# Performance work log

Hardware: AMD Instinct MI355X
Metric: run time of the kernel (lower is better)

The kernel has to match this reference:

```python
import jax, jax.numpy as jnp
import numpy as np

B, V, S, H = 16384, 16, 64, 512


def setup_inputs() -> dict:
    key = jax.random.key(0)
    kx, kw, kb, kws, kbs = jax.random.split(key, 5)
    x = jax.random.normal(kx, (B, V, S), dtype=jnp.float32)
    # per-variable linear layers: weight [V, S, H], bias [V, H]
    W = jax.random.normal(kw, (V, S, H), dtype=jnp.float32) * (1.0 / np.sqrt(S))
    b = jax.random.normal(kb, (V, H), dtype=jnp.float32) * 0.01
    # variable selection linear: hidden -> V
    W_sel = jax.random.normal(kws, (H, V), dtype=jnp.float32) * (1.0 / np.sqrt(H))
    b_sel = jax.random.normal(kbs, (V,), dtype=jnp.float32) * 0.01
    return {"x": x, "W": W, "b": b, "W_sel": W_sel, "b_sel": b_sel}


def reference(x, W, b, W_sel, b_sel):
    # per-variable linears: [B, V, H]
    transformed = jnp.einsum('bvs,vsh->bvh', x, W) + b  # grouped small GEMMs
    # torch stacks to [B, H, V]; mean over variable axis -> [B, H]
    flat = transformed.mean(axis=1)
    # softmax-gated selection weights [B, V] (dropout is identity in eval)
    weights = jax.nn.softmax(flat @ W_sel + b_sel, axis=-1)
    # weighted sum over variables -> [B, H]
    out = jnp.einsum('bvh,bv->bh', transformed, weights)
    return out
```

## Files before the change

kernel.cpp:

```cpp
#include <hip/hip_runtime.h>
#include <hip/hip_bf16.h>
#include <stdint.h>

#define B_ROWS 16384
#define VDIM   16
#define SDIM   64
#define HDIM   512
#define KDIM   1024
#define KP     1056

using bf16x8 = __attribute__((ext_vector_type(8))) __bf16;
using u16x8  = __attribute__((ext_vector_type(8))) unsigned short;
using f32x4  = __attribute__((ext_vector_type(4))) float;

__device__ __forceinline__ unsigned short f2bf(float f) {
  unsigned int u = __builtin_bit_cast(unsigned int, f);
  u = (u + 0x7FFFu + ((u >> 16) & 1u)) >> 16;
  return (unsigned short)u;
}

__device__ __forceinline__ void gl_lds16(const void* g, void* l) {
  __builtin_amdgcn_global_load_lds(
      (const __attribute__((address_space(1))) void*)(g),
      (__attribute__((address_space(3))) void*)(l),
      16, 0, 0);
}

__global__ __launch_bounds__(256) void k0a_build_bt(
    const float* __restrict__ W, const float* __restrict__ bias,
    unsigned short* __restrict__ Bt) {
  int idx = blockIdx.x * 256 + threadIdx.x;
  if (idx >= KP * HDIM) return;
  int k = idx >> 9;
  int n = idx & 511;
  float val;
  if (k < KDIM)            val = W[(size_t)k * HDIM + n];
  else if (k < KDIM + 16)  val = bias[(size_t)(k - KDIM) * HDIM + n];
  else                     val = 0.f;
  Bt[(size_t)n * KP + k] = f2bf(val);
}

__global__ __launch_bounds__(256) void k0b_comb(
    const float* __restrict__ W, const float* __restrict__ bias,
    const float* __restrict__ Wsel, const float* __restrict__ bsel,
    unsigned short* __restrict__ WcombT, float* __restrict__ bcomb) {
  __shared__ float wsl[512 * 17];
  __shared__ float bm[HDIM];
  __shared__ float part[16][17];
  const int t = threadIdx.x;
  if (blockIdx.x < 256) {
    for (int i = t; i < 512 * 16; i += 256) {
      int h = i >> 4, v = i & 15;
      wsl[h * 17 + v] = Wsel[i];
    }
    __syncthreads();
    const int wave = t >> 6, lane = t & 63;
    const int k = blockIdx.x * 4 + wave;
    const float* wr = W + (size_t)k * HDIM;
    float s[16];
    #pragma unroll
    for (int v = 0; v < 16; ++v) s[v] = 0.f;
    #pragma unroll
    for (int j = 0; j < 8; ++j) {
      const int h = lane + 64 * j;
      const float a = wr[h];
      const float* wl = &wsl[h * 17];
      #pragma unroll
      for (int v = 0; v < 16; ++v) s[v] = fmaf(a, wl[v], s[v]);
    }
    #pragma unroll
    for (int off = 32; off > 0; off >>= 1) {
      #pragma unroll
      for (int v = 0; v < 16; ++v) s[v] += __shfl_xor(s[v], off, 64);
    }
    float mine = 0.f;
    #pragma unroll
    for (int v = 0; v < 16; ++v) mine = (lane == v) ? s[v] : mine;
    if (lane < 16) WcombT[lane * KDIM + k] = f2bf(mine * (1.f / 16.f));
  } else {
    for (int h = t; h < HDIM; h += 256) {
      float s = 0.f;
      #pragma unroll
      for (int v = 0; v < VDIM; ++v) s += bias[v * HDIM + h];
      bm[h] = s * (1.f / 16.f);
    }
    __syncthreads();
    int v = t & 15, sl = t >> 4;
    float s = 0.f;
    for (int h = sl * 32; h < sl * 32 + 32; ++h) s = fmaf(bm[h], Wsel[h * VDIM + v], s);
    part[sl][v] = s;
    __syncthreads();
    if (t < 16) {
      float s2 = bsel[t];
      #pragma unroll
      for (int i = 0; i < 16; ++i) s2 += part[i][t];
      bcomb[t] = s2;
    }
  }
}

__global__ __launch_bounds__(256) void k1a_logits(
    const float* __restrict__ x, const unsigned short* __restrict__ WcombT,
    float* __restrict__ part) {
  const int gw = blockIdx.x * 4 + (threadIdx.x >> 6);
  const int lane = threadIdx.x & 63;
  const int rt = gw >> 2, seg = gw & 3;
  const int m = lane & 15, quad = lane >> 4;
  const float* xr = x + (size_t)(rt * 16 + m) * KDIM + seg * 256 + quad * 8;
  const unsigned short* br = WcombT + m * KDIM + seg * 256 + quad * 8;
  f32x4 acc = {0.f, 0.f, 0.f, 0.f};
  #pragma unroll
  for (int kt = 0; kt < 8; ++kt) {
    float4 a0 = *(const float4*)(xr);
    float4 a1 = *(const float4*)(xr + 4);
    xr += 32;
    u16x8 u;
    u[0] = f2bf(a0.x); u[1] = f2bf(a0.y); u[2] = f2bf(a0.z); u[3] = f2bf(a0.w);
    u[4] = f2bf(a1.x); u[5] = f2bf(a1.y); u[6] = f2bf(a1.z); u[7] = f2bf(a1.w);
    bf16x8 af = __builtin_bit_cast(bf16x8, u);
    bf16x8 bfv = *(const bf16x8*)(br);
    br += 32;
    acc = __builtin_amdgcn_mfma_f32_16x16x32_bf16(af, bfv, acc, 0, 0, 0);
  }
  float* pr = part + (size_t)(rt * 16 + quad * 4) * 64 + seg * 16 + m;
  #pragma unroll
  for (int r = 0; r < 4; ++r) pr[(size_t)r * 64] = acc[r];
}

__global__ __launch_bounds__(256) void k1b0_softmax(
    const float* __restrict__ part, const float* __restrict__ bcomb,
    float* __restrict__ weights, unsigned short* __restrict__ Ax) {
  const int row = blockIdx.x * 256 + threadIdx.x;
  const float* p = part + (size_t)row * 64;
  float l[16];
  float mx = -1e30f;
  #pragma unroll
  for (int v = 0; v < 16; ++v) {
    l[v] = bcomb[v] + p[v] + p[16 + v] + p[32 + v] + p[48 + v];
    mx = fmaxf(mx, l[v]);
  }
  float s = 0.f;
  #pragma unroll
  for (int v = 0; v < 16; ++v) { l[v] = __expf(l[v] - mx); s += l[v]; }
  const float inv = 1.f / s;
  float4* wout = (float4*)(weights + (size_t)row * 16);
  #pragma unroll
  for (int q = 0; q < 4; ++q) {
    float4 f;
    f.x = l[4 * q + 0] * inv; f.y = l[4 * q + 1] * inv;
    f.z = l[4 * q + 2] * inv; f.w = l[4 * q + 3] * inv;
    wout[q] = f;
  }
  unsigned short tb[16];
  #pragma unroll
  for (int v = 0; v < 16; ++v) tb[v] = f2bf(l[v] * inv);
  uint4* tp = (uint4*)(Ax + (size_t)row * KP + KDIM);
  tp[0] = *(const uint4*)(&tb[0]);
  tp[1] = *(const uint4*)(&tb[8]);
  uint4 z; z.x = 0; z.y = 0; z.z = 0; z.w = 0;
  tp[2] = z;
  tp[3] = z;
}

__global__ __launch_bounds__(256) void k1b_scale(
    const float* __restrict__ x, const float* __restrict__ weights,
    unsigned short* __restrict__ Ax) {
  const int wave = threadIdx.x >> 6, lane = threadIdx.x & 63;
  #pragma unroll
  for (int r = 0; r < 2; ++r) {
    const int row = blockIdx.x * 8 + wave * 2 + r;
    const float w = weights[(size_t)row * 16 + (lane >> 2)];
    const float4* xr = (const float4*)(x + (size_t)row * KDIM + lane * 16);
    float4 v0 = xr[0], v1 = xr[1], v2 = xr[2], v3 = xr[3];
    unsigned short o[16];
    o[0]  = f2bf(w * v0.x); o[1]  = f2bf(w * v0.y); o[2]  = f2bf(w * v0.z); o[3]  = f2bf(w * v0.w);
    o[4]  = f2bf(w * v1.x); o[5]  = f2bf(w * v1.y); o[6]  = f2bf(w * v1.z); o[7]  = f2bf(w * v1.w);
    o[8]  = f2bf(w * v2.x); o[9]  = f2bf(w * v2.y); o[10] = f2bf(w * v2.z); o[11] = f2bf(w * v2.w);
    o[12] = f2bf(w * v3.x); o[13] = f2bf(w * v3.y); o[14] = f2bf(w * v3.z); o[15] = f2bf(w * v3.w);
    uint4* yp = (uint4*)(Ax + (size_t)row * KP + lane * 16);
    yp[0] = *(const uint4*)(&o[0]);
    yp[1] = *(const uint4*)(&o[8]);
  }
}

__global__ __launch_bounds__(256) void k2_gemm(
    const unsigned short* __restrict__ A, const unsigned short* __restrict__ Bt,
    float* __restrict__ C) {
  __shared__ unsigned short As[128 * 32];
  __shared__ unsigned short Bs[128 * 32];

  const int t = threadIdx.x;
  const int wave = t >> 6, lane = t & 63;
  const int tm = blockIdx.x >> 2, tn = blockIdx.x & 3;
  const int mlane = lane & 15, quad = lane >> 4;
  const int RM = (wave >> 1) * 64, CN = (wave & 1) * 64;

  const int srow = lane >> 2;
  const int scol = (lane & 3) * 8;
  const int c0 = wave * 2;
  const unsigned short* ag0 = A  + (size_t)(tm * 128 + (c0 + 0) * 16 + srow) * KP + scol;
  const unsigned short* ag1 = A  + (size_t)(tm * 128 + (c0 + 1) * 16 + srow) * KP + scol;
  const unsigned short* bg0 = Bt + (size_t)(tn * 128 + (c0 + 0) * 16 + srow) * KP + scol;
  const unsigned short* bg1 = Bt + (size_t)(tn * 128 + (c0 + 1) * 16 + srow) * KP + scol;
  unsigned short* asd0 = &As[(c0 + 0) * 512];
  unsigned short* asd1 = &As[(c0 + 1) * 512];
  unsigned short* bsd0 = &Bs[(c0 + 0) * 512];
  unsigned short* bsd1 = &Bs[(c0 + 1) * 512];

  const unsigned short* ap[4];
  const unsigned short* bp[4];
  #pragma unroll
  for (int i = 0; i < 4; ++i) {
    ap[i] = &As[(RM + i * 16 + mlane) * 32 + quad * 8];
    bp[i] = &Bs[(CN + i * 16 + mlane) * 32 + quad * 8];
  }

  f32x4 acc[4][4];
  const f32x4 z = {0.f, 0.f, 0.f, 0.f};
  #pragma unroll
  for (int i = 0; i < 4; ++i)
    #pragma unroll
    for (int j = 0; j < 4; ++j) acc[i][j] = z;

  for (int kt = 0; kt < KP / 32; ++kt) {
    gl_lds16(ag0, asd0); gl_lds16(ag1, asd1);
    gl_lds16(bg0, bsd0); gl_lds16(bg1, bsd1);
    ag0 += 32; ag1 += 32; bg0 += 32; bg1 += 32;
    __syncthreads();
    bf16x8 af[4], bfv[4];
    #pragma unroll
    for (int i = 0; i < 4; ++i) af[i]  = *(const bf16x8*)ap[i];
    #pragma unroll
    for (int j = 0; j < 4; ++j) bfv[j] = *(const bf16x8*)bp[j];
    #pragma unroll
    for (int i = 0; i < 4; ++i)
      #pragma unroll
      for (int j = 0; j < 4; ++j)
        acc[i][j] = __builtin_amdgcn_mfma_f32_16x16x32_bf16(af[i], bfv[j], acc[i][j], 0, 0, 0);
    __syncthreads();
  }

  const size_t rowb = (size_t)(tm * 128 + RM);
  const int colb = tn * 128 + CN;
  #pragma unroll
  for (int i = 0; i < 4; ++i)
    #pragma unroll
    for (int j = 0; j < 4; ++j)
      #pragma unroll
      for (int r = 0; r < 4; ++r) {
        const size_t row = rowb + i * 16 + quad * 4 + r;
        const int col = colb + j * 16 + mlane;
        C[row * HDIM + col] = acc[i][j][r];
      }
}

extern "C" void kernel_launch(void* const* d_in, const int* in_sizes, int n_in,
                              void* d_out, int out_size, void* d_ws, size_t ws_size,
                              hipStream_t stream) {
  const float* x    = (const float*)d_in[0];
  const float* W    = (const float*)d_in[1];
  const float* bias = (const float*)d_in[2];
  const float* Wsel = (const float*)d_in[3];
  const float* bsel = (const float*)d_in[4];
  float* out = (float*)d_out;

  char* ws = (char*)d_ws;
  unsigned short* Bt     = (unsigned short*)(ws);
  unsigned short* WcombT = (unsigned short*)(ws + 1081344);
  float*          bcomb  = (float*)(ws + 1114112);
  float*          part   = (float*)(ws + 1114368);
  float*          wts    = (float*)(ws + 5308672);
  unsigned short* Ax     = (unsigned short*)(ws + 6357248);

  k0a_build_bt<<<2112, 256, 0, stream>>>(W, bias, Bt);
  k0b_comb<<<257, 256, 0, stream>>>(W, bias, Wsel, bsel, WcombT, bcomb);
  k1a_logits<<<1024, 256, 0, stream>>>(x, WcombT, part);
  k1b0_softmax<<<64, 256, 0, stream>>>(part, bcomb, wts, Ax);
  k1b_scale<<<2048, 256, 0, stream>>>(x, wts, Ax);
  k2_gemm<<<512, 256, 0, stream>>>(Ax, Bt, out);
}
```

Before: 171.5 us.

## Fuse weight scaling and bf16 conversion into GEMM A-tile load, merge prep kernels

The GEMM now reads fp32 x and the softmax weights directly. It scales and converts each A tile to bf16 in registers before staging it in LDS, which removes the separate scale kernel and the Ax intermediate buffer. The GEMM M tile shrinks to 64 rows, giving twice as many blocks, and the B tile gets an XOR swizzle to avoid LDS bank conflicts. The two weight-prep kernels are merged into a single launch. The trade-off is that A loads become synchronous register loads rather than direct-to-LDS, each x tile is re-read for every N tile, and the fused conversion adds ALU work inside the main loop.

```diff
diff --git a/kernel.cpp b/kernel.cpp
--- a/kernel.cpp
+++ b/kernel.cpp
@@ -26,36 +26,35 @@
       16, 0, 0);
 }
 
-__global__ __launch_bounds__(256) void k0a_build_bt(
-    const float* __restrict__ W, const float* __restrict__ bias,
-    unsigned short* __restrict__ Bt) {
-  int idx = blockIdx.x * 256 + threadIdx.x;
-  if (idx >= KP * HDIM) return;
-  int k = idx >> 9;
-  int n = idx & 511;
-  float val;
-  if (k < KDIM)            val = W[(size_t)k * HDIM + n];
-  else if (k < KDIM + 16)  val = bias[(size_t)(k - KDIM) * HDIM + n];
-  else                     val = 0.f;
-  Bt[(size_t)n * KP + k] = f2bf(val);
-}
-
-__global__ __launch_bounds__(256) void k0b_comb(
+__global__ __launch_bounds__(256) void k0_prep(
     const float* __restrict__ W, const float* __restrict__ bias,
     const float* __restrict__ Wsel, const float* __restrict__ bsel,
-    unsigned short* __restrict__ WcombT, float* __restrict__ bcomb) {
+    unsigned short* __restrict__ Bt, unsigned short* __restrict__ WcombT,
+    float* __restrict__ bcomb) {
   __shared__ float wsl[512 * 17];
   __shared__ float bm[HDIM];
   __shared__ float part[16][17];
   const int t = threadIdx.x;
-  if (blockIdx.x < 256) {
+  if (blockIdx.x < 2112) {
+    int idx = blockIdx.x * 256 + t;
+    int k = idx >> 9;
+    int n = idx & 511;
+    float val;
+    if (k < KDIM)            val = W[(size_t)k * HDIM + n];
+    else if (k < KDIM + 16)  val = bias[(size_t)(k - KDIM) * HDIM + n];
+    else                     val = 0.f;
+    Bt[(size_t)n * KP + k] = f2bf(val);
+    return;
+  }
+  const int bid = blockIdx.x - 2112;
+  if (bid < 256) {
     for (int i = t; i < 512 * 16; i += 256) {
       int h = i >> 4, v = i & 15;
       wsl[h * 17 + v] = Wsel[i];
     }
     __syncthreads();
     const int wave = t >> 6, lane = t & 63;
-    const int k = blockIdx.x * 4 + wave;
+    const int k = bid * 4 + wave;
     const float* wr = W + (size_t)k * HDIM;
     float s[16];
     #pragma unroll
@@ -129,7 +128,7 @@
 
 __global__ __launch_bounds__(256) void k1b0_softmax(
     const float* __restrict__ part, const float* __restrict__ bcomb,
-    float* __restrict__ weights, unsigned short* __restrict__ Ax) {
+    float* __restrict__ weights) {
   const int row = blockIdx.x * 256 + threadIdx.x;
   const float* p = part + (size_t)row * 64;
   float l[16];
@@ -151,99 +150,99 @@
     f.z = l[4 * q + 2] * inv; f.w = l[4 * q + 3] * inv;
     wout[q] = f;
   }
-  unsigned short tb[16];
-  #pragma unroll
-  for (int v = 0; v < 16; ++v) tb[v] = f2bf(l[v] * inv);
-  uint4* tp = (uint4*)(Ax + (size_t)row * KP + KDIM);
-  tp[0] = *(const uint4*)(&tb[0]);
-  tp[1] = *(const uint4*)(&tb[8]);
-  uint4 z; z.x = 0; z.y = 0; z.z = 0; z.w = 0;
-  tp[2] = z;
-  tp[3] = z;
-}
-
-__global__ __launch_bounds__(256) void k1b_scale(
-    const float* __restrict__ x, const float* __restrict__ weights,
-    unsigned short* __restrict__ Ax) {
-  const int wave = threadIdx.x >> 6, lane = threadIdx.x & 63;
-  #pragma unroll
-  for (int r = 0; r < 2; ++r) {
-    const int row = blockIdx.x * 8 + wave * 2 + r;
-    const float w = weights[(size_t)row * 16 + (lane >> 2)];
-    const float4* xr = (const float4*)(x + (size_t)row * KDIM + lane * 16);
-    float4 v0 = xr[0], v1 = xr[1], v2 = xr[2], v3 = xr[3];
-    unsigned short o[16];
-    o[0]  = f2bf(w * v0.x); o[1]  = f2bf(w * v0.y); o[2]  = f2bf(w * v0.z); o[3]  = f2bf(w * v0.w);
-    o[4]  = f2bf(w * v1.x); o[5]  = f2bf(w * v1.y); o[6]  = f2bf(w * v1.z); o[7]  = f2bf(w * v1.w);
-    o[8]  = f2bf(w * v2.x); o[9]  = f2bf(w * v2.y); o[10] = f2bf(w * v2.z); o[11] = f2bf(w * v2.w);
-    o[12] = f2bf(w * v3.x); o[13] = f2bf(w * v3.y); o[14] = f2bf(w * v3.z); o[15] = f2bf(w * v3.w);
-    uint4* yp = (uint4*)(Ax + (size_t)row * KP + lane * 16);
-    yp[0] = *(const uint4*)(&o[0]);
-    yp[1] = *(const uint4*)(&o[8]);
-  }
-}
-
-__global__ __launch_bounds__(256) void k2_gemm(
-    const unsigned short* __restrict__ A, const unsigned short* __restrict__ Bt,
-    float* __restrict__ C) {
-  __shared__ unsigned short As[128 * 32];
+}
+
+__global__ __launch_bounds__(256, 4) void k2f_gemm(
+    const float* __restrict__ x, const float* __restrict__ wts,
+    const unsigned short* __restrict__ Bt, float* __restrict__ C) {
+  __shared__ unsigned short As[64 * 40];
   __shared__ unsigned short Bs[128 * 32];
 
   const int t = threadIdx.x;
   const int wave = t >> 6, lane = t & 63;
   const int tm = blockIdx.x >> 2, tn = blockIdx.x & 3;
   const int mlane = lane & 15, quad = lane >> 4;
-  const int RM = (wave >> 1) * 64, CN = (wave & 1) * 64;
-
-  const int srow = lane >> 2;
-  const int scol = (lane & 3) * 8;
+  const int wr = wave >> 1, wc = wave & 1;
+
+  const int arow = t >> 2;
+  const int kq = (t & 3) * 8;
+  const int grow = tm * 64 + arow;
+  const float* xrow = x + (size_t)grow * KDIM + kq;
+  const float* wrow = wts + (size_t)grow * 16;
+  unsigned short* asw = &As[arow * 40 + kq];
+
   const int c0 = wave * 2;
-  const unsigned short* ag0 = A  + (size_t)(tm * 128 + (c0 + 0) * 16 + srow) * KP + scol;
-  const unsigned short* ag1 = A  + (size_t)(tm * 128 + (c0 + 1) * 16 + srow) * KP + scol;
-  const unsigned short* bg0 = Bt + (size_t)(tn * 128 + (c0 + 0) * 16 + srow) * KP + scol;
-  const unsigned short* bg1 = Bt + (size_t)(tn * 128 + (c0 + 1) * 16 + srow) * KP + scol;
-  unsigned short* asd0 = &As[(c0 + 0) * 512];
-  unsigned short* asd1 = &As[(c0 + 1) * 512];
-  unsigned short* bsd0 = &Bs[(c0 + 0) * 512];
-  unsigned short* bsd1 = &Bs[(c0 + 1) * 512];
-
-  const unsigned short* ap[4];
+  const int nrow = lane >> 2;
+  const int ksw = ((lane & 3) ^ (nrow & 3)) * 8;
+  const unsigned short* bg0 = Bt + (size_t)(tn * 128 + (c0 + 0) * 16 + nrow) * KP + ksw;
+  const unsigned short* bg1 = Bt + (size_t)(tn * 128 + (c0 + 1) * 16 + nrow) * KP + ksw;
+  unsigned short* bsd0 = &Bs[(c0 + 0) * 16 * 32];
+  unsigned short* bsd1 = &Bs[(c0 + 1) * 16 * 32];
+
+  const unsigned short* ap[2];
+  #pragma unroll
+  for (int i = 0; i < 2; ++i)
+    ap[i] = &As[(wr * 32 + i * 16 + mlane) * 40 + quad * 8];
   const unsigned short* bp[4];
   #pragma unroll
-  for (int i = 0; i < 4; ++i) {
-    ap[i] = &As[(RM + i * 16 + mlane) * 32 + quad * 8];
-    bp[i] = &Bs[(CN + i * 16 + mlane) * 32 + quad * 8];
-  }
-
-  f32x4 acc[4][4];
+  for (int j = 0; j < 4; ++j) {
+    const int nl = wc * 64 + j * 16 + mlane;
+    bp[j] = &Bs[nl * 32 + ((quad ^ (mlane & 3)) * 8)];
+  }
+
+  f32x4 acc[2][4];
   const f32x4 z = {0.f, 0.f, 0.f, 0.f};
   #pragma unroll
-  for (int i = 0; i < 4; ++i)
+  for (int i = 0; i < 2; ++i)
     #pragma unroll
     for (int j = 0; j < 4; ++j) acc[i][j] = z;
 
-  for (int kt = 0; kt < KP / 32; ++kt) {
-    gl_lds16(ag0, asd0); gl_lds16(ag1, asd1);
-    gl_lds16(bg0, bsd0); gl_lds16(bg1, bsd1);
-    ag0 += 32; ag1 += 32; bg0 += 32; bg1 += 32;
-    __syncthreads();
-    bf16x8 af[4], bfv[4];
-    #pragma unroll
-    for (int i = 0; i < 4; ++i) af[i]  = *(const bf16x8*)ap[i];
+  for (int kt = 0; kt < 33; ++kt) {
+    gl_lds16(bg0, bsd0);
+    gl_lds16(bg1, bsd1);
+    bg0 += 32; bg1 += 32;
+    float vals[8];
+    if (kt < 32) {
+      const float4 a0 = *(const float4*)(xrow);
+      const float4 a1 = *(const float4*)(xrow + 4);
+      xrow += 32;
+      const float w = wrow[kt >> 1];
+      vals[0] = w * a0.x; vals[1] = w * a0.y; vals[2] = w * a0.z; vals[3] = w * a0.w;
+      vals[4] = w * a1.x; vals[5] = w * a1.y; vals[6] = w * a1.z; vals[7] = w * a1.w;
+    } else {
+      if (kq < 16) {
+        const float4 w0 = *(const float4*)(wrow + kq);
+        const float4 w1 = *(const float4*)(wrow + kq + 4);
+        vals[0] = w0.x; vals[1] = w0.y; vals[2] = w0.z; vals[3] = w0.w;
+        vals[4] = w1.x; vals[5] = w1.y; vals[6] = w1.z; vals[7] = w1.w;
+      } else {
+        #pragma unroll
+        for (int j = 0; j < 8; ++j) vals[j] = 0.f;
+      }
+    }
+    u16x8 u;
+    #pragma unroll
+    for (int j = 0; j < 8; ++j) u[j] = f2bf(vals[j]);
+    *(u16x8*)asw = u;
+
+    __syncthreads();
+    bf16x8 af[2], bfv[4];
+    #pragma unroll
+    for (int i = 0; i < 2; ++i) af[i]  = *(const bf16x8*)ap[i];
     #pragma unroll
     for (int j = 0; j < 4; ++j) bfv[j] = *(const bf16x8*)bp[j];
     #pragma unroll
-    for (int i = 0; i < 4; ++i)
+    for (int i = 0; i < 2; ++i)
       #pragma unroll
       for (int j = 0; j < 4; ++j)
         acc[i][j] = __builtin_amdgcn_mfma_f32_16x16x32_bf16(af[i], bfv[j], acc[i][j], 0, 0, 0);
     __syncthreads();
   }
 
-  const size_t rowb = (size_t)(tm * 128 + RM);
-  const int colb = tn * 128 + CN;
-  #pragma unroll
-  for (int i = 0; i < 4; ++i)
+  const size_t rowb = (size_t)(tm * 64 + wr * 32);
+  const int colb = tn * 128 + wc * 64;
+  #pragma unroll
+  for (int i = 0; i < 2; ++i)
     #pragma unroll
     for (int j = 0; j < 4; ++j)
       #pragma unroll
@@ -270,12 +269,9 @@
   float*          bcomb  = (float*)(ws + 1114112);
   float*          part   = (float*)(ws + 1114368);
   float*          wts    = (float*)(ws + 5308672);
-  unsigned short* Ax     = (unsigned short*)(ws + 6357248);
-
-  k0a_build_bt<<<2112, 256, 0, stream>>>(W, bias, Bt);
-  k0b_comb<<<257, 256, 0, stream>>>(W, bias, Wsel, bsel, WcombT, bcomb);
+
+  k0_prep<<<2369, 256, 0, stream>>>(W, bias, Wsel, bsel, Bt, WcombT, bcomb);
   k1a_logits<<<1024, 256, 0, stream>>>(x, WcombT, part);
-  k1b0_softmax<<<64, 256, 0, stream>>>(part, bcomb, wts, Ax);
-  k1b_scale<<<2048, 256, 0, stream>>>(x, wts, Ax);
-  k2_gemm<<<512, 256, 0, stream>>>(Ax, Bt, out);
-}
+  k1b0_softmax<<<64, 256, 0, stream>>>(part, bcomb, wts);
+  k2f_gemm<<<1024, 256, 0, stream>>>(x, wts, Bt, out);
+}
```

Measured after the change: 182.9 us. +6.6%, slower.
